# Optimization experiments

Measured on AMD Instinct MI355X. Metric: run time of the kernel, lower is better.

## Reference

```python
import jax, jax.numpy as jnp
import numpy as np

B, S, D, F, E, K, R, H = 4, 1024, 1024, 512, 8, 2, 64, 256
TEMP = 1.0          # step=0 -> 0.5+0.5*cos(0)=1.0, clamp(min=0.1) -> 1.0
BW, EW, ZW = 0.3, 0.1, 1e-4


def fq(t):
    """Per-tensor symmetric int8 fake-quant with straight-through estimator."""
    s = jnp.maximum(jnp.max(jnp.abs(t)) / 127.0, 1e-8)
    q = jnp.clip(jnp.round(t / s), -128, 127) * s
    return t + jax.lax.stop_gradient(q - t)


def lora_lin(h, W, A, Bm):
    # base weight is frozen (requires_grad=False) and fake-quantized
    y = h @ fq(jax.lax.stop_gradient(W)).T + (h @ Bm.T) @ A.T
    return fq(y)


def ffn(h, w1, a1, b1, w2, a2, b2, w3, a3, b3):
    # use_swiglu=True path: gate = sigmoid(w3(x)); out = w2(w1(x)*gate); dropout=eval identity
    gate = jax.nn.sigmoid(lora_lin(h, w3, a3, b3))
    out = lora_lin(lora_lin(h, w1, a1, b1) * gate, w2, a2, b2)
    return fq(out)


def setup_inputs() -> dict:
    key = jax.random.key(0)
    k = jax.random.split(key, 32)
    n = lambda i, shp: jax.random.normal(k[i], shp, dtype=jnp.float32) * 0.02
    return {
        "x": jax.random.normal(k[0], (B, S, D), dtype=jnp.float32),
        "scorer_w": n(1, (E, D)), "scorer_b": jnp.zeros((E,), jnp.float32),
        "p1_w": n(2, (H, D)), "p1_b": jnp.zeros((H,), jnp.float32),
        "p2_w": n(3, (E, H)), "p2_b": jnp.zeros((E,), jnp.float32),
        "ew1_w": n(4, (E, F, D)), "ew1_a": n(5, (E, F, R)), "ew1_b": n(6, (E, R, D)),
        "ew2_w": n(7, (E, D, F)), "ew2_a": n(8, (E, D, R)), "ew2_b": n(9, (E, R, F)),
        "ew3_w": n(10, (E, F, D)), "ew3_a": n(11, (E, F, R)), "ew3_b": n(12, (E, R, D)),
        "s1_w": n(13, (F, D)), "s1_a": n(14, (F, R)), "s1_b": n(15, (R, D)),
        "s2_w": n(16, (D, F)), "s2_a": n(17, (D, R)), "s2_b": n(18, (R, F)),
        "s3_w": n(19, (F, D)), "s3_a": n(20, (F, R)), "s3_b": n(21, (R, D)),
    }


def reference(x, scorer_w, scorer_b, p1_w, p1_b, p2_w, p2_b,
              ew1_w, ew1_a, ew1_b, ew2_w, ew2_a, ew2_b, ew3_w, ew3_a, ew3_b,
              s1_w, s1_a, s1_b, s2_w, s2_a, s2_b, s3_w, s3_a, s3_b):
    xf = x.reshape(-1, D)                                           # [T, D]
    # --- router (per-token) ---
    base = (xf @ scorer_w.T + scorer_b) / TEMP                      # [T, E]
    policy = jax.nn.softmax(jax.nn.relu(xf @ p1_w.T + p1_b) @ p2_w.T + p2_b, axis=-1)
    scores = jax.nn.softmax((base + policy) * 0.5, axis=-1)         # fp32 softmax
    entropy = -(scores * jnp.log(scores + 1e-6)).sum(-1).mean()
    z_loss = ZW * (jax.nn.logsumexp(base, axis=-1) ** 2).mean()
    weights, indices = jax.lax.top_k(scores, K)                     # [T, K]
    weights = weights * TEMP
    cw = (jax.nn.one_hot(indices, E, dtype=weights.dtype) * weights[..., None]).sum(1)  # [T, E]
    usage = cw.sum(0)                                               # [E]
    uf = usage / (usage.mean() + 1e-6)
    balance_loss = BW * jnp.var(uf, ddof=1) - EW * entropy + z_loss
    # --- expert dispatch: dense masked combine (faithful to weighted scatter-add) ---
    eout = jax.vmap(lambda w1, a1, b1, w2, a2, b2, w3, a3, b3:
                    ffn(xf, w1, a1, b1, w2, a2, b2, w3, a3, b3))(
        ew1_w, ew1_a, ew1_b, ew2_w, ew2_a, ew2_b, ew3_w, ew3_a, ew3_b)  # [E, T, D]
    y = jnp.einsum('te,etd->td', cw, eout)                          # weighted combine
    z = ffn(xf, s1_w, s1_a, s1_b, s2_w, s2_a, s2_b, s3_w, s3_a, s3_b)
    out = (y + z).reshape(x.shape)
    return (out, usage, balance_loss, jnp.float32(0.0), jnp.float32(0.0))
```

## Files before the change

### kernel.cpp

```cpp
#include <hip/hip_runtime.h>

#define TTOK 4096
#define DDIM 1024
#define FDIM 512
#define NEXP 8
#define HDIM 256
#define RLORA 64
#define CROWS 14336

using u16 = unsigned short;
using f4v = __attribute__((ext_vector_type(4))) float;
using bfrag = __attribute__((ext_vector_type(8))) short;
using u16x8 = __attribute__((ext_vector_type(8))) unsigned short;

static __device__ __forceinline__ float bf2f(u16 u) {
  union { unsigned int u; float f; } x; x.u = ((unsigned int)u) << 16; return x.f;
}
static __device__ __forceinline__ u16 f2bf(float f) {
  union { float f; unsigned int u; } x; x.f = f;
  unsigned int r = (x.u + 0x7fffu + ((x.u >> 16) & 1u)) >> 16;
  return (u16)r;
}
static __device__ __forceinline__ float fq1(float t, float s) {
  float q = rintf(t / s);
  q = fminf(fmaxf(q, -128.f), 127.f);
  return q * s;
}

struct GemmGArgs {
  const u16* A; const u16* B; u16* C;
  const int* tokmap; const int2* blkmap; const int* nbrow;
};

#define STAGE1(d, kt, h, l) \
  __builtin_amdgcn_global_load_lds( \
    (const __attribute__((address_space(1))) void*)(gs[(h)*2+(l)] + (size_t)(kt)*64), \
    (__attribute__((address_space(3))) void*)&lds[(d)*32768 + (h)*8192 + (tid + (l)*512)*8], \
    16, 0, 0)

template <int MODE>
__global__ __launch_bounds__(512, 2) void gemm256g(GemmGArgs g) {
  const int br = blockIdx.x;
  if (br >= g.nbrow[0]) return;
  const int2 bm = g.blkmap[br];
  const int e = bm.x;
  const int m0 = bm.y;
  const int n0 = blockIdx.y * 256;
  const int tid = threadIdx.x;
  const int lane = tid & 63;
  const int wave = tid >> 6;
  const int wr = wave >> 2;
  const int wc = wave & 3;

  constexpr int K = MODE ? 1024 : 512;
  const u16* Bp = g.B + (size_t)e * (MODE ? 1048576 : 524288);

  __shared__ u16 lds[65536];

  const u16* gs[8];
#pragma unroll
  for (int h = 0; h < 4; h++)
#pragma unroll
    for (int l = 0; l < 2; l++) {
      const int slot = tid + l * 512;
      const int row = slot >> 3, p = slot & 7;
      const int glog = p ^ (row & 7);
      const u16* basep;
      if (h < 2) {
        const int grow = m0 + h * 128 + row;
        const int t = MODE ? g.tokmap[grow] : grow;
        basep = g.A + (size_t)t * K;
      } else {
        basep = Bp + (size_t)(n0 + (h - 2) * 128 + row) * K;
      }
      gs[h * 2 + l] = basep + glog * 8;
    }

  f4v acc[8][4];
#pragma unroll
  for (int i = 0; i < 8; i++)
#pragma unroll
    for (int j = 0; j < 4; j++) acc[i][j] = (f4v){0.f, 0.f, 0.f, 0.f};

  const int q = lane >> 4;
  const int lx = lane & 7;
  const int l15 = lane & 15;

#pragma unroll
  for (int h = 0; h < 4; h++) { STAGE1(0, 0, h, 0); STAGE1(0, 0, h, 1); }
  __syncthreads();

  constexpr int nt = K >> 6;
  for (int kt = 0; kt < nt; ++kt) {
    const int d = kt & 1;
    const int dn = d ^ 1;
    const bool more = (kt + 1 < nt);
#pragma unroll
    for (int kk = 0; kk < 2; ++kk) {
      if (more) {
        if (kk == 0) { STAGE1(dn, kt + 1, 0, 0); STAGE1(dn, kt + 1, 0, 1);
                       STAGE1(dn, kt + 1, 1, 0); STAGE1(dn, kt + 1, 1, 1); }
        else         { STAGE1(dn, kt + 1, 2, 0); STAGE1(dn, kt + 1, 2, 1);
                       STAGE1(dn, kt + 1, 3, 0); STAGE1(dn, kt + 1, 3, 1); }
      }
      bfrag afr[8], bfr[4];
      const int pa = ((kk * 4 + q) ^ lx) << 3;
      const int abase = d * 32768 + wr * 8192 + l15 * 64 + pa;
#pragma unroll
      for (int mi = 0; mi < 8; mi++) afr[mi] = *(const bfrag*)&lds[abase + mi * 1024];
      const int bbase = d * 32768 + (2 + (wc >> 1)) * 8192 + (((wc & 1) << 6) + l15) * 64 + pa;
#pragma unroll
      for (int ni = 0; ni < 4; ni++) bfr[ni] = *(const bfrag*)&lds[bbase + ni * 1024];
      __builtin_amdgcn_s_setprio(1);
#pragma unroll
      for (int mi = 0; mi < 8; mi++)
#pragma unroll
        for (int ni = 0; ni < 4; ni++)
          acc[mi][ni] = __builtin_amdgcn_mfma_f32_16x16x32_bf16(afr[mi], bfr[ni], acc[mi][ni], 0, 0, 0);
      __builtin_amdgcn_s_setprio(0);
    }
    __syncthreads();
  }

  const int crow0 = m0 + wr * 128 + q * 4;

  if (MODE == 1) {
    float* xlds = (float*)lds;
    const int lrow0 = wr * 128 + q * 4;
    if (wc >= 2) {
      const int lc = (wc - 2) * 64 + l15;
#pragma unroll
      for (int mi = 0; mi < 8; mi++)
#pragma unroll
        for (int ni = 0; ni < 4; ni++)
#pragma unroll
          for (int r = 0; r < 4; r++)
            xlds[(lrow0 + mi * 16 + r) * 128 + lc + ni * 16] = acc[mi][ni][r];
    }
    __syncthreads();
    if (wc < 2) {
      const int lc = wc * 64 + l15;
      const int fbase = (n0 >> 1) + lc;
#pragma unroll
      for (int mi = 0; mi < 8; mi++)
#pragma unroll
        for (int r = 0; r < 4; r++) {
          const int rowg = crow0 + mi * 16 + r;
          const int lr = lrow0 + mi * 16 + r;
#pragma unroll
          for (int ni = 0; ni < 4; ni++) {
            float y1 = acc[mi][ni][r];
            float y3 = xlds[lr * 128 + lc + ni * 16];
            float h = y1 / (1.f + __expf(-y3));
            g.C[(size_t)rowg * FDIM + fbase + ni * 16] = f2bf(h);
          }
        }
    }
  } else {
    const int ccol0 = n0 + wc * 64 + l15;
#pragma unroll
    for (int mi = 0; mi < 8; mi++)
#pragma unroll
      for (int ni = 0; ni < 4; ni++) {
        const int col = ccol0 + ni * 16;
#pragma unroll
        for (int r = 0; r < 4; r++)
          g.C[(size_t)(crow0 + mi * 16 + r) * 1024 + col] = f2bf(acc[mi][ni][r]);
      }
  }
}

struct MidArgs {
  const u16* A64; const u16* B64; u16* C64; const float* bias64;
  const u16* A0; const u16* B0;
  const u16* Wb;
  u16* C13; u16* C2e;
  const float* amaxP;
};

__global__ __launch_bounds__(256) void mid_kernel(MidArgs g) {
  __shared__ u16 smem[25600];
  __shared__ float s_sw;
  const int bid = blockIdx.x;
  const int tid = threadIdx.x;
  const int lane = tid & 63;
  const int wave = tid >> 6;

  if (bid < 256) {
    const int wr = wave >> 1, wc = wave & 1;
    const int m0 = (bid & 63) * 64, n0 = (bid >> 6) * 64;
    const int K = DDIM, N = HDIM;
    u16* As = smem;
    u16* Bs = smem + 2048;

    const int ldrow = tid >> 2;
    const int swzcol = (((tid & 3) ^ ((tid >> 3) & 3)) << 3);
    const u16* ga = g.A64 + (size_t)(m0 + ldrow) * K + swzcol;
    const u16* gb = g.B64 + (size_t)(n0 + ldrow) * K + swzcol;

    f4v acc[2][2];
#pragma unroll
    for (int i = 0; i < 2; i++)
#pragma unroll
      for (int j = 0; j < 2; j++) acc[i][j] = (f4v){0.f, 0.f, 0.f, 0.f};

    const int rbase = lane & 15;
    const int q = lane >> 4;
    const int pg = (q ^ ((rbase >> 1) & 3)) << 3;
    const int arow = (wr << 5) + rbase;
    const int brow = (wc << 5) + rbase;

    for (int kt = 0; kt < K; kt += 32) {
      __builtin_amdgcn_global_load_lds((const __attribute__((address_space(1))) void*)(ga),
          (__attribute__((address_space(3))) void*)&As[tid * 8], 16, 0, 0);
      __builtin_amdgcn_global_load_lds((const __attribute__((address_space(1))) void*)(gb),
          (__attribute__((address_space(3))) void*)&Bs[tid * 8], 16, 0, 0);
      ga += 32; gb += 32;
      __syncthreads();
      bfrag af[2], bf[2];
#pragma unroll
      for (int mi = 0; mi < 2; mi++)
        af[mi] = *(const bfrag*)&As[(arow + mi * 16) * 32 + pg];
#pragma unroll
      for (int ni = 0; ni < 2; ni++)
        bf[ni] = *(const bfrag*)&Bs[(brow + ni * 16) * 32 + pg];
#pragma unroll
      for (int mi = 0; mi < 2; mi++)
#pragma unroll
        for (int ni = 0; ni < 2; ni++)
          acc[mi][ni] = __builtin_amdgcn_mfma_f32_16x16x32_bf16(af[mi], bf[ni], acc[mi][ni], 0, 0, 0);
      __syncthreads();
    }

    const int crow0 = m0 + (wr << 5) + ((lane >> 4) << 2);
    const int ccol0 = n0 + (wc << 5) + (lane & 15);
#pragma unroll
    for (int mi = 0; mi < 2; mi++)
#pragma unroll
      for (int ni = 0; ni < 2; ni++) {
        const int n = ccol0 + ni * 16;
        const float b = g.bias64[n];
#pragma unroll
        for (int r = 0; r < 4; r++) {
          float v = fmaxf(acc[mi][ni][r] + b, 0.f);
          g.C64[(size_t)(crow0 + mi * 16 + r) * N + n] = f2bf(v);
        }
      }
    return;
  }

  const int fid = bid - 256;
  const int z = fid >> 6;
  const int rem = fid & 63;
  const int bx = rem & 7, by = rem >> 3;
  const bool is13 = z < 18;
  if (is13 ? (bx >= 4) : (by >= 4)) return;
  const int N = is13 ? 1024 : 512;
  const int K = 64;
  const u16* Ap = is13 ? g.A0 + (size_t)z * 32768 : g.A0 + 589824 + (size_t)(z - 18) * 65536;
  const u16* Bp = is13 ? g.B0 + (size_t)z * 65536 : g.B0 + 1179648 + (size_t)(z - 18) * 32768;
  const u16* Wf = g.Wb + (size_t)z * 524288;
  u16* Cb; int flag;
  if (is13) {
    const int slot = (z >= 16) ? 8 : (z & 7);
    Cb = g.C13 + (size_t)slot * 1048576;
    flag = (z >= 8 && z < 16) || z == 17 ? 2 : 1;
  } else {
    Cb = g.C2e + (size_t)(z - 18) * 524288;
    flag = 0;
  }

  const int wr = wave >> 1, wc = wave & 1;
  const int m0 = bx * 128, n0 = by * 128;
  u16* As = smem;
  u16* Bs = smem + 4096;
  u16* stage = smem + 8192;

  if (wave == 0) {
    float m = fmaxf(g.amaxP[z * 128 + lane], g.amaxP[z * 128 + 64 + lane]);
#pragma unroll
    for (int off = 32; off > 0; off >>= 1) m = fmaxf(m, __shfl_xor(m, off));
    if (lane == 0) s_sw = fmaxf(m / 127.f, 1e-8f);
  }

  const int ldrow = tid >> 2;
  const int swzcol = (((tid & 3) ^ ((tid >> 3) & 3)) << 3);
  const u16* ga = Ap + (size_t)(m0 + ldrow) * K + swzcol;
  const u16* gb = Bp + (size_t)(n0 + ldrow) * K + swzcol;
  const size_t rowstep = (size_t)64 * K;

  f4v acc[4][4];
#pragma unroll
  for (int i = 0; i < 4; i++)
#pragma unroll
    for (int j = 0; j < 4; j++) acc[i][j] = (f4v){0.f, 0.f, 0.f, 0.f};

  const int rbase = lane & 15;
  const int q = lane >> 4;
  const int pg = (q ^ ((rbase >> 1) & 3)) << 3;
  const int arow = (wr << 6) + rbase;
  const int brow = (wc << 6) + rbase;

  for (int kt = 0; kt < K; kt += 32) {
    __builtin_amdgcn_global_load_lds((const __attribute__((address_space(1))) void*)(ga),
        (__attribute__((address_space(3))) void*)&As[tid * 8], 16, 0, 0);
    __builtin_amdgcn_global_load_lds((const __attribute__((address_space(1))) void*)(ga + rowstep),
        (__attribute__((address_space(3))) void*)&As[(256 + tid) * 8], 16, 0, 0);
    __builtin_amdgcn_global_load_lds((const __attribute__((address_space(1))) void*)(gb),
        (__attribute__((address_space(3))) void*)&Bs[tid * 8], 16, 0, 0);
    __builtin_amdgcn_global_load_lds((const __attribute__((address_space(1))) void*)(gb + rowstep),
        (__attribute__((address_space(3))) void*)&Bs[(256 + tid) * 8], 16, 0, 0);
    ga += 32; gb += 32;
    __syncthreads();
    bfrag af[4], bf[4];
#pragma unroll
    for (int mi = 0; mi < 4; mi++)
      af[mi] = *(const bfrag*)&As[(arow + mi * 16) * 32 + pg];
#pragma unroll
    for (int ni = 0; ni < 4; ni++)
      bf[ni] = *(const bfrag*)&Bs[(brow + ni * 16) * 32 + pg];
#pragma unroll
    for (int mi = 0; mi < 4; mi++)
#pragma unroll
      for (int ni = 0; ni < 4; ni++)
        acc[mi][ni] = __builtin_amdgcn_mfma_f32_16x16x32_bf16(af[mi], bf[ni], acc[mi][ni], 0, 0, 0);
    __syncthreads();
  }

  const int lrow0 = (wr << 6) + ((lane >> 4) << 2);
  const int lcol0 = (wc << 6) + (lane & 15);
#pragma unroll
  for (int mi = 0; mi < 4; mi++)
#pragma unroll
    for (int ni = 0; ni < 4; ni++) {
      const int n = lcol0 + ni * 16;
#pragma unroll
      for (int r = 0; r < 4; r++)
        stage[(lrow0 + mi * 16 + r) * 136 + n] = f2bf(acc[mi][ni][r]);
    }
  __syncthreads();
  const float sw = s_sw;

  const int dm0 = flag ? (((m0 >> 7) << 8) + (flag == 2 ? 128 : 0)) : m0;
#pragma unroll
  for (int j = 0; j < 8; j++) {
    const int s = j * 256 + tid;
    const int lr = s >> 4;
    const int n8 = (s & 15) << 3;
    const u16x8 wv = *(const u16x8*)&Wf[(size_t)(m0 + lr) * N + n0 + n8];
    const bfrag sv = *(const bfrag*)&stage[lr * 136 + n8];
    u16x8 o;
#pragma unroll
    for (int k = 0; k < 8; k++)
      o[k] = f2bf(fq1(bf2f(wv[k]), sw) + bf2f((u16)sv[k]));
    *(u16x8*)&Cb[(size_t)(dm0 + lr) * N + n0 + n8] = o;
  }
}

struct PrepArgs {
  const float* W[27]; u16* Wraw; float* amaxP;
  const float* xf; u16* xfb;
  const float* p1w; u16* p1wb;
  const float* Asrc[27]; u16* Adst;
  const float* Bsrc[27]; u16* Bdst;
};
__global__ __launch_bounds__(256) void prep_kernel(PrepArgs a) {
  const int bid = blockIdx.x;
  const int tid = threadIdx.x;
  if (bid < 3456) {
    const int t = bid >> 7;
    const int bx = bid & 127;
    const float4* src = (const float4*)a.W[t];
    ushort4* dst = (ushort4*)(a.Wraw + (size_t)t * 524288);
    const int i0 = bx * 256 + tid;
    float4 v0 = src[i0];
    float4 v1 = src[i0 + 32768];
    float4 v2 = src[i0 + 65536];
    float4 v3 = src[i0 + 98304];
    ushort4 o0, o1, o2, o3;
    o0.x = f2bf(v0.x); o0.y = f2bf(v0.y); o0.z = f2bf(v0.z); o0.w = f2bf(v0.w);
    o1.x = f2bf(v1.x); o1.y = f2bf(v1.y); o1.z = f2bf(v1.z); o1.w = f2bf(v1.w);
    o2.x = f2bf(v2.x); o2.y = f2bf(v2.y); o2.z = f2bf(v2.z); o2.w = f2bf(v2.w);
    o3.x = f2bf(v3.x); o3.y = f2bf(v3.y); o3.z = f2bf(v3.z); o3.w = f2bf(v3.w);
    dst[i0] = o0; dst[i0 + 32768] = o1; dst[i0 + 65536] = o2; dst[i0 + 98304] = o3;
    float m01 = fmaxf(fmaxf(fabsf(v0.x), fabsf(v0.y)), fmaxf(fabsf(v0.z), fabsf(v0.w)));
    float m11 = fmaxf(fmaxf(fabsf(v1.x), fabsf(v1.y)), fmaxf(fabsf(v1.z), fabsf(v1.w)));
    float m21 = fmaxf(fmaxf(fabsf(v2.x), fabsf(v2.y)), fmaxf(fabsf(v2.z), fabsf(v2.w)));
    float m31 = fmaxf(fmaxf(fabsf(v3.x), fabsf(v3.y)), fmaxf(fabsf(v3.z), fabsf(v3.w)));
    float lmax = fmaxf(fmaxf(m01, m11), fmaxf(m21, m31));
#pragma unroll
    for (int off = 32; off > 0; off >>= 1) lmax = fmaxf(lmax, __shfl_xor(lmax, off));
    __shared__ float wm[4];
    if ((tid & 63) == 0) wm[tid >> 6] = lmax;
    __syncthreads();
    if (tid == 0)
      a.amaxP[t * 128 + bx] = fmaxf(fmaxf(wm[0], wm[1]), fmaxf(wm[2], wm[3]));
    return;
  }
  const int cid = bid - 3456;
  const int slice = cid >> 10;
  const int g0 = (cid & 1023) * 256 + tid;
  const int stride = 262144;
  if (slice == 0) {
    for (int i = g0; i < 1048576; i += stride) {
      float4 v = ((const float4*)a.xf)[i];
      ushort4 o; o.x = f2bf(v.x); o.y = f2bf(v.y); o.z = f2bf(v.z); o.w = f2bf(v.w);
      ((ushort4*)a.xfb)[i] = o;
    }
  } else if (slice == 1) {
    for (int i = g0; i < 65536; i += stride) {
      float4 v = ((const float4*)a.p1w)[i];
      ushort4 o; o.x = f2bf(v.x); o.y = f2bf(v.y); o.z = f2bf(v.z); o.w = f2bf(v.w);
      ((ushort4*)a.p1wb)[i] = o;
    }
  } else if (slice == 2) {
    for (int i = g0; i < 1179648; i += stride) {
      int t, off;
      if (i < 589824) { t = i >> 15; off = i & 32767; }
      else { int j = i - 589824; t = 18 + (j >> 16); off = j & 65535; }
      a.Adst[i] = f2bf(a.Asrc[t][off]);
    }
  } else {
    for (int i = g0; i < 1474560; i += stride) {
      int t, src;
      if (i < 1179648) { t = i >> 16; int off = i & 65535; src = (off & 63) * 1024 + (off >> 6); }
      else { int j = i - 1179648; t = 18 + (j >> 15); int off = j & 32767; src = (off & 63) * 512 + (off >> 6); }
      a.Bdst[i] = f2bf(a.Bsrc[t][src]);
    }
  }
}

struct RouterArgs {
  const float* xf; const u16* ph;
  const float* sw; const float* sb;
  const float* p2w; const float* p2b;
  float* base; float* pol;
};
__global__ __launch_bounds__(256) void router_small(RouterArgs a) {
  __shared__ float sw[8][1024];
  __shared__ float p2[8][256];
  const int tid = threadIdx.x;
  {
    const float4* s0 = (const float4*)a.sw;
    float4* d0 = (float4*)&sw[0][0];
    for (int i = tid; i < 2048; i += 256) d0[i] = s0[i];
    const float4* s1 = (const float4*)a.p2w;
    float4* d1 = (float4*)&p2[0][0];
    for (int i = tid; i < 512; i += 256) d1[i] = s1[i];
  }
  __syncthreads();
  const int tl = tid >> 4, s = tid & 15;
  const int token = blockIdx.x * 16 + tl;
  float acc[8] = {0,0,0,0,0,0,0,0}, pacc[8] = {0,0,0,0,0,0,0,0};
  const float4* xrow = (const float4*)(a.xf + (size_t)token * 1024);
  for (int i = 0; i < 16; i++) {
    const int d4 = i * 16 + s;
    float4 xv = xrow[d4];
#pragma unroll
    for (int e = 0; e < 8; e++) {
      float4 wv = ((const float4*)&sw[e][0])[d4];
      acc[e] += xv.x * wv.x + xv.y * wv.y + xv.z * wv.z + xv.w * wv.w;
    }
  }
  const u16* phrow = a.ph + (size_t)token * 256;
  for (int i = 0; i < 16; i++) {
    const int h = i * 16 + s;
    float pv = bf2f(phrow[h]);
#pragma unroll
    for (int e = 0; e < 8; e++) pacc[e] += pv * p2[e][h];
  }
#pragma unroll
  for (int off = 8; off > 0; off >>= 1)
#pragma unroll
    for (int e = 0; e < 8; e++) {
      acc[e] += __shfl_xor(acc[e], off);
      pacc[e] += __shfl_xor(pacc[e], off);
    }
  if (s == 0) {
#pragma unroll
    for (int e = 0; e < 8; e++) {
      a.base[token * 8 + e] = acc[e] + a.sb[e];
      a.pol[token * 8 + e] = pacc[e] + a.p2b[e];
    }
  }
}

struct FinArgs {
  const float* base; const float* pol;
  float* partials;
  int* idx2; float2* wb; int* histArr;
};
__global__ __launch_bounds__(256) void router_topk(FinArgs a) {
  const int tid = threadIdx.x;
  const int lane = tid & 63, wv = tid >> 6;
  const int token = blockIdx.x * 256 + tid;
  float b[8], p[8];
#pragma unroll
  for (int e = 0; e < 8; e++) { b[e] = a.base[token * 8 + e]; p[e] = a.pol[token * 8 + e]; }
  float pm = p[0];
#pragma unroll
  for (int e = 1; e < 8; e++) pm = fmaxf(pm, p[e]);
  float pe[8], psum = 0.f;
#pragma unroll
  for (int e = 0; e < 8; e++) { pe[e] = expf(p[e] - pm); psum += pe[e]; }
  const float pinv = 1.f / psum;
  float sl[8];
#pragma unroll
  for (int e = 0; e < 8; e++) sl[e] = (b[e] + pe[e] * pinv) * 0.5f;
  float sm = sl[0];
#pragma unroll
  for (int e = 1; e < 8; e++) sm = fmaxf(sm, sl[e]);
  float sc[8], ssum = 0.f;
#pragma unroll
  for (int e = 0; e < 8; e++) { sc[e] = expf(sl[e] - sm); ssum += sc[e]; }
  const float sinv = 1.f / ssum;
  float ent = 0.f;
#pragma unroll
  for (int e = 0; e < 8; e++) { float v = sc[e] * sinv; sc[e] = v; ent -= v * logf(v + 1e-6f); }
  float bm = b[0];
#pragma unroll
  for (int e = 1; e < 8; e++) bm = fmaxf(bm, b[e]);
  float zs = 0.f;
#pragma unroll
  for (int e = 0; e < 8; e++) zs += expf(b[e] - bm);
  const float lse = logf(zs) + bm;
  const float zt = lse * lse;
  float m1 = -1e30f, m2 = -1e30f; int i1 = 0, i2 = 0;
#pragma unroll
  for (int e = 0; e < 8; e++) {
    float v = sc[e];
    if (v > m1) { m2 = m1; i2 = i1; m1 = v; i1 = e; }
    else if (v > m2) { m2 = v; i2 = e; }
  }
  a.idx2[token] = i1 | (i2 << 8);
  a.wb[token] = make_float2(m1, m2);

  __shared__ int hist[8];
  if (tid < 8) hist[tid] = 0;
  __syncthreads();
  atomicAdd(&hist[i1], 1);
  atomicAdd(&hist[i2], 1);
  __syncthreads();
  if (tid < 8) a.histArr[blockIdx.x * 8 + tid] = hist[tid];

  float vals[10];
  vals[0] = ent; vals[1] = zt;
#pragma unroll
  for (int e = 0; e < 8; e++) vals[2 + e] = 0.f;
  vals[2 + i1] = m1; vals[2 + i2] = m2;
#pragma unroll
  for (int v = 0; v < 10; v++)
#pragma unroll
    for (int off = 32; off > 0; off >>= 1) vals[v] += __shfl_down(vals[v], off);
  __shared__ float wred[4][10];
  if (lane == 0)
#pragma unroll
    for (int v = 0; v < 10; v++) wred[wv][v] = vals[v];
  __syncthreads();
  if (tid < 10)
    a.partials[blockIdx.x * 10 + tid] = wred[0][tid] + wred[1][tid] + wred[2][tid] + wred[3][tid];
}

__global__ __launch_bounds__(256) void compact_setup(const int* idx2, const int* histArr,
                                                     int2* blkmap, int* nbrow, int* tokmap,
                                                     int* posb, const float* partials, float* tail) {
  const int e = blockIdx.x;
  const int tid = threadIdx.x;
  int cntl[8];
#pragma unroll
  for (int i = 0; i < 8; i++) {
    int s = 0;
    for (int bblk = 0; bblk < 16; bblk++) s += histArr[bblk * 8 + i];
    cntl[i] = s;
  }
  if (e == 8) {
    if (tid == 0) {
      int o = 0, nb = 16;
      for (int i = 0; i < 16; i++) blkmap[i] = make_int2(8, i * 256);
      for (int ex = 0; ex < 8; ex++) {
        const int nbe = (cntl[ex] + 255) >> 8;
        for (int i = 0; i < nbe; i++) blkmap[nb++] = make_int2(ex, 4096 + o + i * 256);
        o += nbe << 8;
      }
      nbrow[0] = nb;
    } else if (tid == 64) {
      float ent = 0.f, z = 0.f, us[8] = {0,0,0,0,0,0,0,0};
      for (int i = 0; i < 16; i++) {
        ent += partials[i * 10 + 0];
        z += partials[i * 10 + 1];
        for (int ex = 0; ex < 8; ex++) us[ex] += partials[i * 10 + 2 + ex];
      }
      float tot = 0.f;
      for (int ex = 0; ex < 8; ex++) tot += us[ex];
      const float meanu = tot / 8.f;
      float uf[8], mu = 0.f;
      for (int ex = 0; ex < 8; ex++) { uf[ex] = us[ex] / (meanu + 1e-6f); mu += uf[ex]; }
      mu /= 8.f;
      float var = 0.f;
      for (int ex = 0; ex < 8; ex++) { float d = uf[ex] - mu; var += d * d; }
      var /= 7.f;
      const float bl = 0.3f * var - 0.1f * (ent / 4096.f) + 1e-4f * (z / 4096.f);
      for (int ex = 0; ex < 8; ex++) tail[ex] = us[ex];
      tail[8] = bl; tail[9] = 0.f; tail[10] = 0.f;
    }
    for (int t = tid; t < 4096; t += 256) tokmap[t] = t;
    return;
  }
  const int lane = tid & 63, wv = tid >> 6;
  __shared__ int wtot[4];
  __shared__ int carry;
  if (tid == 0) carry = 0;
  __syncthreads();
  int off = 0;
  for (int i = 0; i < e; i++) off += ((cntl[i] + 255) >> 8) << 8;
  const int base = 4096 + off;
  for (int c = 0; c < 16; c++) {
    const int t = c * 256 + tid;
    const int ii = idx2[t];
    const int i1 = ii & 255, i2 = ii >> 8;
    const int flag = (i1 == e || i2 == e) ? 1 : 0;
    const unsigned long long m = __ballot(flag);
    const int pre = __popcll(m & ((1ull << lane) - 1ull));
    if (lane == 63) wtot[wv] = pre + flag;
    __syncthreads();
    int wbase = 0;
    for (int i = 0; i < wv; i++) wbase += wtot[i];
    if (flag) {
      const int row = base + carry + wbase + pre;
      tokmap[row] = t;
      posb[t * 2 + (i2 == e ? 1 : 0)] = row;
    }
    __syncthreads();
    if (tid == 0) carry += wtot[0] + wtot[1] + wtot[2] + wtot[3];
    __syncthreads();
  }
  const int ce = cntl[e];
  const int pend = ((ce + 255) >> 8) << 8;
  for (int r = ce + tid; r < pend; r += 256) tokmap[base + r] = 0;
}

__global__ __launch_bounds__(256) void combine_g(const u16* y2c, const int* posb,
                                                 const float2* wb, float* out) {
  const int t = blockIdx.x;
  const int c = threadIdx.x;
  const float2 w = wb[t];
  const int p1 = posb[t * 2], p2 = posb[t * 2 + 1];
  ushort4 s = ((const ushort4*)(y2c + (size_t)t * 1024))[c];
  ushort4 a = ((const ushort4*)(y2c + (size_t)p1 * 1024))[c];
  ushort4 b = ((const ushort4*)(y2c + (size_t)p2 * 1024))[c];
  float4 o;
  o.x = bf2f(s.x) + w.x * bf2f(a.x) + w.y * bf2f(b.x);
  o.y = bf2f(s.y) + w.x * bf2f(a.y) + w.y * bf2f(b.y);
  o.z = bf2f(s.z) + w.x * bf2f(a.z) + w.y * bf2f(b.z);
  o.w = bf2f(s.w) + w.x * bf2f(a.w) + w.y * bf2f(b.w);
  ((float4*)(out + (size_t)t * 1024))[c] = o;
}

extern "C" void kernel_launch(void* const* d_in, const int* in_sizes, int n_in,
                              void* d_out, int out_size, void* d_ws, size_t ws_size,
                              hipStream_t stream) {
  const float* x = (const float*)d_in[0];
  const float* scorer_w = (const float*)d_in[1];
  const float* scorer_b = (const float*)d_in[2];
  const float* p1_w = (const float*)d_in[3];
  const float* p1_b = (const float*)d_in[4];
  const float* p2_w = (const float*)d_in[5];
  const float* p2_b = (const float*)d_in[6];
  const float* ew1_w = (const float*)d_in[7];
  const float* ew1_a = (const float*)d_in[8];
  const float* ew1_b = (const float*)d_in[9];
  const float* ew2_w = (const float*)d_in[10];
  const float* ew2_a = (const float*)d_in[11];
  const float* ew2_b = (const float*)d_in[12];
  const float* ew3_w = (const float*)d_in[13];
  const float* ew3_a = (const float*)d_in[14];
  const float* ew3_b = (const float*)d_in[15];
  const float* s1_w = (const float*)d_in[16];
  const float* s1_a = (const float*)d_in[17];
  const float* s1_b = (const float*)d_in[18];
  const float* s2_w = (const float*)d_in[19];
  const float* s2_a = (const float*)d_in[20];
  const float* s2_b = (const float*)d_in[21];
  const float* s3_w = (const float*)d_in[22];
  const float* s3_a = (const float*)d_in[23];
  const float* s3_b = (const float*)d_in[24];
  float* outf = (float*)d_out;

  char* w = (char*)d_ws;
  auto alloc = [&](size_t bytes) { char* p = w; w += (bytes + 255) & ~(size_t)255; return p; };
  u16* xfb  = (u16*)alloc((size_t)TTOK * DDIM * 2);
  u16* ph   = (u16*)alloc((size_t)TTOK * HDIM * 2);
  u16* p1wb = (u16*)alloc((size_t)HDIM * DDIM * 2);
  u16* Adst = (u16*)alloc((size_t)1179648 * 2);
  u16* Bdst = (u16*)alloc((size_t)1474560 * 2);
  u16* Wraw = (u16*)alloc((size_t)27 * 524288 * 2);
  u16* W13  = (u16*)alloc((size_t)9 * 1024 * 1024 * 2);
  u16* W2e  = (u16*)alloc((size_t)9 * 1024 * 512 * 2);
  u16* h2c  = (u16*)alloc((size_t)CROWS * FDIM * 2);
  u16* y2c  = (u16*)alloc((size_t)CROWS * DDIM * 2);
  float* base = (float*)alloc((size_t)TTOK * 8 * 4);
  float* pol  = (float*)alloc((size_t)TTOK * 8 * 4);
  float* partials = (float*)alloc(16 * 10 * 4);
  float* amaxP = (float*)alloc(27 * 128 * 4);
  int* histArr = (int*)alloc(16 * 8 * 4);
  int2* blkmap = (int2*)alloc(64 * 8);
  int* nbrow  = (int*)alloc(4);
  int* tokmap = (int*)alloc(CROWS * 4);
  int* posb   = (int*)alloc(TTOK * 2 * 4);
  int* idx2   = (int*)alloc(TTOK * 4);
  float2* wb  = (float2*)alloc(TTOK * 8);

  {
    PrepArgs a{};
    for (int e = 0; e < 8; e++) {
      a.W[e] = ew1_w + (size_t)e * 524288;
      a.W[8 + e] = ew3_w + (size_t)e * 524288;
      a.W[18 + e] = ew2_w + (size_t)e * 524288;
      a.Asrc[e] = ew1_a + (size_t)e * 32768;
      a.Asrc[8 + e] = ew3_a + (size_t)e * 32768;
      a.Asrc[18 + e] = ew2_a + (size_t)e * 65536;
      a.Bsrc[e] = ew1_b + (size_t)e * 65536;
      a.Bsrc[8 + e] = ew3_b + (size_t)e * 65536;
      a.Bsrc[18 + e] = ew2_b + (size_t)e * 32768;
    }
    a.W[16] = s1_w; a.W[17] = s3_w; a.W[26] = s2_w;
    a.Asrc[16] = s1_a; a.Asrc[17] = s3_a; a.Asrc[26] = s2_a;
    a.Bsrc[16] = s1_b; a.Bsrc[17] = s3_b; a.Bsrc[26] = s2_b;
    a.Wraw = Wraw; a.amaxP = amaxP;
    a.xf = x; a.xfb = xfb; a.p1w = p1_w; a.p1wb = p1wb;
    a.Adst = Adst; a.Bdst = Bdst;
    hipLaunchKernelGGL(prep_kernel, dim3(7552), dim3(256), 0, stream, a);
  }
  {
    MidArgs g{};
    g.A64 = xfb; g.B64 = p1wb; g.C64 = ph; g.bias64 = p1_b;
    g.A0 = Adst; g.B0 = Bdst; g.Wb = Wraw; g.C13 = W13; g.C2e = W2e; g.amaxP = amaxP;
    hipLaunchKernelGGL(mid_kernel, dim3(1984), dim3(256), 0, stream, g);
  }
  {
    RouterArgs r{};
    r.xf = x; r.ph = ph; r.sw = scorer_w; r.sb = scorer_b;
    r.p2w = p2_w; r.p2b = p2_b; r.base = base; r.pol = pol;
    hipLaunchKernelGGL(router_small, dim3(256), dim3(256), 0, stream, r);
  }
  {
    FinArgs f{base, pol, partials, idx2, wb, histArr};
    hipLaunchKernelGGL(router_topk, dim3(16), dim3(256), 0, stream, f);
  }
  hipLaunchKernelGGL(compact_setup, dim3(9), dim3(256), 0, stream,
                     idx2, histArr, blkmap, nbrow, tokmap, posb, partials,
                     outf + (size_t)TTOK * DDIM);
  {
    GemmGArgs g{xfb, W13, h2c, tokmap, blkmap, nbrow};
    hipLaunchKernelGGL(gemm256g<1>, dim3(56, 4), dim3(512), 0, stream, g);
  }
  {
    GemmGArgs g{h2c, W2e, y2c, tokmap, blkmap, nbrow};
    hipLaunchKernelGGL(gemm256g<0>, dim3(56, 4), dim3(512), 0, stream, g);
  }
  hipLaunchKernelGGL(combine_g, dim3(4096), dim3(256), 0, stream, y2c, posb, wb, outf);
}
```

Baseline: 153.3 us.

## Fuse router kernels, remap GEMM block order, stage gate tile in bf16

Merges the router logit kernel and the top-k/softmax kernel into one launch. Logits now stay in shared memory, which drops the base/pol global round trip and one kernel launch. In exchange, the partial sums and histograms grow to 256 blocks, so compact_setup reduces more entries. The GEMMs use a 1D grid with a remapped block order so that the four column tiles of a row block land on the same XCD, aiming at better L2 reuse. The gate tile staged in LDS becomes bf16 with a padded stride of 136, which halves LDS traffic but rounds the gate logits to bf16 before the sigmoid.

Result: slower. 222.0 us (+44.7%).

```diff
diff --git a/kernel.cpp b/kernel.cpp
--- a/kernel.cpp
+++ b/kernel.cpp
@@ -40,12 +40,14 @@
 
 template <int MODE>
 __global__ __launch_bounds__(512, 2) void gemm256g(GemmGArgs g) {
-  const int br = blockIdx.x;
+  const int bid = blockIdx.x;
+  const int logical = (bid & 7) * 28 + (bid >> 3);
+  const int br = logical >> 2;
   if (br >= g.nbrow[0]) return;
   const int2 bm = g.blkmap[br];
   const int e = bm.x;
   const int m0 = bm.y;
-  const int n0 = blockIdx.y * 256;
+  const int n0 = (logical & 3) * 256;
   const int tid = threadIdx.x;
   const int lane = tid & 63;
   const int wave = tid >> 6;
@@ -125,7 +127,7 @@
   const int crow0 = m0 + wr * 128 + q * 4;
 
   if (MODE == 1) {
-    float* xlds = (float*)lds;
+    u16* stage = lds;
     const int lrow0 = wr * 128 + q * 4;
     if (wc >= 2) {
       const int lc = (wc - 2) * 64 + l15;
@@ -135,7 +137,7 @@
         for (int ni = 0; ni < 4; ni++)
 #pragma unroll
           for (int r = 0; r < 4; r++)
-            xlds[(lrow0 + mi * 16 + r) * 128 + lc + ni * 16] = acc[mi][ni][r];
+            stage[(lrow0 + mi * 16 + r) * 136 + lc + ni * 16] = f2bf(acc[mi][ni][r]);
     }
     __syncthreads();
     if (wc < 2) {
@@ -150,7 +152,7 @@
 #pragma unroll
           for (int ni = 0; ni < 4; ni++) {
             float y1 = acc[mi][ni][r];
-            float y3 = xlds[lr * 128 + lc + ni * 16];
+            float y3 = bf2f(stage[lr * 136 + lc + ni * 16]);
             float h = y1 / (1.f + __expf(-y3));
             g.C[(size_t)rowg * FDIM + fbase + ni * 16] = f2bf(h);
           }
@@ -434,11 +436,16 @@
   const float* xf; const u16* ph;
   const float* sw; const float* sb;
   const float* p2w; const float* p2b;
-  float* base; float* pol;
+  int* idx2; float2* wb;
+  float* partials;
+  int* histArr;
 };
-__global__ __launch_bounds__(256) void router_small(RouterArgs a) {
+__global__ __launch_bounds__(256) void router_kernel(RouterArgs a) {
   __shared__ float sw[8][1024];
   __shared__ float p2[8][256];
+  __shared__ float blog[16][8];
+  __shared__ float plog[16][8];
+  __shared__ int hist[8];
   const int tid = threadIdx.x;
   {
     const float4* s0 = (const float4*)a.sw;
@@ -448,117 +455,106 @@
     float4* d1 = (float4*)&p2[0][0];
     for (int i = tid; i < 512; i += 256) d1[i] = s1[i];
   }
+  if (tid < 8) hist[tid] = 0;
   __syncthreads();
   const int tl = tid >> 4, s = tid & 15;
   const int token = blockIdx.x * 16 + tl;
-  float acc[8] = {0,0,0,0,0,0,0,0}, pacc[8] = {0,0,0,0,0,0,0,0};
-  const float4* xrow = (const float4*)(a.xf + (size_t)token * 1024);
-  for (int i = 0; i < 16; i++) {
-    const int d4 = i * 16 + s;
-    float4 xv = xrow[d4];
+  {
+    float acc[8] = {0,0,0,0,0,0,0,0}, pacc[8] = {0,0,0,0,0,0,0,0};
+    const float4* xrow = (const float4*)(a.xf + (size_t)token * 1024);
+    for (int i = 0; i < 16; i++) {
+      const int d4 = i * 16 + s;
+      float4 xv = xrow[d4];
+#pragma unroll
+      for (int e = 0; e < 8; e++) {
+        float4 wv = ((const float4*)&sw[e][0])[d4];
+        acc[e] += xv.x * wv.x + xv.y * wv.y + xv.z * wv.z + xv.w * wv.w;
+      }
+    }
+    const u16* phrow = a.ph + (size_t)token * 256;
+    for (int i = 0; i < 16; i++) {
+      const int h = i * 16 + s;
+      float pv = bf2f(phrow[h]);
+#pragma unroll
+      for (int e = 0; e < 8; e++) pacc[e] += pv * p2[e][h];
+    }
+#pragma unroll
+    for (int off = 8; off > 0; off >>= 1)
+#pragma unroll
+      for (int e = 0; e < 8; e++) {
+        acc[e] += __shfl_xor(acc[e], off);
+        pacc[e] += __shfl_xor(pacc[e], off);
+      }
+    if (s == 0) {
+#pragma unroll
+      for (int e = 0; e < 8; e++) {
+        blog[tl][e] = acc[e] + a.sb[e];
+        plog[tl][e] = pacc[e] + a.p2b[e];
+      }
+    }
+  }
+  __syncthreads();
+
+  float vals[10];
+#pragma unroll
+  for (int v = 0; v < 10; v++) vals[v] = 0.f;
+  if (tid < 16) {
+    const int tok = blockIdx.x * 16 + tid;
+    float b[8], p[8];
+#pragma unroll
+    for (int e = 0; e < 8; e++) { b[e] = blog[tid][e]; p[e] = plog[tid][e]; }
+    float pm = p[0];
+#pragma unroll
+    for (int e = 1; e < 8; e++) pm = fmaxf(pm, p[e]);
+    float pe[8], psum = 0.f;
+#pragma unroll
+    for (int e = 0; e < 8; e++) { pe[e] = expf(p[e] - pm); psum += pe[e]; }
+    const float pinv = 1.f / psum;
+    float sl[8];
+#pragma unroll
+    for (int e = 0; e < 8; e++) sl[e] = (b[e] + pe[e] * pinv) * 0.5f;
+    float sm = sl[0];
+#pragma unroll
+    for (int e = 1; e < 8; e++) sm = fmaxf(sm, sl[e]);
+    float sc[8], ssum = 0.f;
+#pragma unroll
+    for (int e = 0; e < 8; e++) { sc[e] = expf(sl[e] - sm); ssum += sc[e]; }
+    const float sinv = 1.f / ssum;
+    float ent = 0.f;
+#pragma unroll
+    for (int e = 0; e < 8; e++) { float v = sc[e] * sinv; sc[e] = v; ent -= v * logf(v + 1e-6f); }
+    float bm = b[0];
+#pragma unroll
+    for (int e = 1; e < 8; e++) bm = fmaxf(bm, b[e]);
+    float zs = 0.f;
+#pragma unroll
+    for (int e = 0; e < 8; e++) zs += expf(b[e] - bm);
+    const float lse = logf(zs) + bm;
+    float m1 = -1e30f, m2 = -1e30f; int i1 = 0, i2 = 0;
 #pragma unroll
     for (int e = 0; e < 8; e++) {
-      float4 wv = ((const float4*)&sw[e][0])[d4];
-      acc[e] += xv.x * wv.x + xv.y * wv.y + xv.z * wv.z + xv.w * wv.w;
-    }
-  }
-  const u16* phrow = a.ph + (size_t)token * 256;
-  for (int i = 0; i < 16; i++) {
-    const int h = i * 16 + s;
-    float pv = bf2f(phrow[h]);
-#pragma unroll
-    for (int e = 0; e < 8; e++) pacc[e] += pv * p2[e][h];
-  }
-#pragma unroll
-  for (int off = 8; off > 0; off >>= 1)
-#pragma unroll
-    for (int e = 0; e < 8; e++) {
-      acc[e] += __shfl_xor(acc[e], off);
-      pacc[e] += __shfl_xor(pacc[e], off);
-    }
-  if (s == 0) {
-#pragma unroll
-    for (int e = 0; e < 8; e++) {
-      a.base[token * 8 + e] = acc[e] + a.sb[e];
-      a.pol[token * 8 + e] = pacc[e] + a.p2b[e];
-    }
-  }
-}
-
-struct FinArgs {
-  const float* base; const float* pol;
-  float* partials;
-  int* idx2; float2* wb; int* histArr;
-};
-__global__ __launch_bounds__(256) void router_topk(FinArgs a) {
-  const int tid = threadIdx.x;
-  const int lane = tid & 63, wv = tid >> 6;
-  const int token = blockIdx.x * 256 + tid;
-  float b[8], p[8];
-#pragma unroll
-  for (int e = 0; e < 8; e++) { b[e] = a.base[token * 8 + e]; p[e] = a.pol[token * 8 + e]; }
-  float pm = p[0];
-#pragma unroll
-  for (int e = 1; e < 8; e++) pm = fmaxf(pm, p[e]);
-  float pe[8], psum = 0.f;
-#pragma unroll
-  for (int e = 0; e < 8; e++) { pe[e] = expf(p[e] - pm); psum += pe[e]; }
-  const float pinv = 1.f / psum;
-  float sl[8];
-#pragma unroll
-  for (int e = 0; e < 8; e++) sl[e] = (b[e] + pe[e] * pinv) * 0.5f;
-  float sm = sl[0];
-#pragma unroll
-  for (int e = 1; e < 8; e++) sm = fmaxf(sm, sl[e]);
-  float sc[8], ssum = 0.f;
-#pragma unroll
-  for (int e = 0; e < 8; e++) { sc[e] = expf(sl[e] - sm); ssum += sc[e]; }
-  const float sinv = 1.f / ssum;
-  float ent = 0.f;
-#pragma unroll
-  for (int e = 0; e < 8; e++) { float v = sc[e] * sinv; sc[e] = v; ent -= v * logf(v + 1e-6f); }
-  float bm = b[0];
-#pragma unroll
-  for (int e = 1; e < 8; e++) bm = fmaxf(bm, b[e]);
-  float zs = 0.f;
-#pragma unroll
-  for (int e = 0; e < 8; e++) zs += expf(b[e] - bm);
-  const float lse = logf(zs) + bm;
-  const float zt = lse * lse;
-  float m1 = -1e30f, m2 = -1e30f; int i1 = 0, i2 = 0;
-#pragma unroll
-  for (int e = 0; e < 8; e++) {
-    float v = sc[e];
-    if (v > m1) { m2 = m1; i2 = i1; m1 = v; i1 = e; }
-    else if (v > m2) { m2 = v; i2 = e; }
-  }
-  a.idx2[token] = i1 | (i2 << 8);
-  a.wb[token] = make_float2(m1, m2);
-
-  __shared__ int hist[8];
-  if (tid < 8) hist[tid] = 0;
-  __syncthreads();
-  atomicAdd(&hist[i1], 1);
-  atomicAdd(&hist[i2], 1);
+      float v = sc[e];
+      if (v > m1) { m2 = m1; i2 = i1; m1 = v; i1 = e; }
+      else if (v > m2) { m2 = v; i2 = e; }
+    }
+    a.idx2[tok] = i1 | (i2 << 8);
+    a.wb[tok] = make_float2(m1, m2);
+    atomicAdd(&hist[i1], 1);
+    atomicAdd(&hist[i2], 1);
+    vals[0] = ent; vals[1] = lse * lse;
+    vals[2 + i1] = m1; vals[2 + i2] = m2;
+  }
+  if (tid < 64) {
+#pragma unroll
+    for (int v = 0; v < 10; v++)
+#pragma unroll
+      for (int off = 32; off > 0; off >>= 1) vals[v] += __shfl_down(vals[v], off);
+    if (tid == 0)
+#pragma unroll
+      for (int v = 0; v < 10; v++) a.partials[blockIdx.x * 10 + v] = vals[v];
+  }
   __syncthreads();
   if (tid < 8) a.histArr[blockIdx.x * 8 + tid] = hist[tid];
-
-  float vals[10];
-  vals[0] = ent; vals[1] = zt;
-#pragma unroll
-  for (int e = 0; e < 8; e++) vals[2 + e] = 0.f;
-  vals[2 + i1] = m1; vals[2 + i2] = m2;
-#pragma unroll
-  for (int v = 0; v < 10; v++)
-#pragma unroll
-    for (int off = 32; off > 0; off >>= 1) vals[v] += __shfl_down(vals[v], off);
-  __shared__ float wred[4][10];
-  if (lane == 0)
-#pragma unroll
-    for (int v = 0; v < 10; v++) wred[wv][v] = vals[v];
-  __syncthreads();
-  if (tid < 10)
-    a.partials[blockIdx.x * 10 + tid] = wred[0][tid] + wred[1][tid] + wred[2][tid] + wred[3][tid];
 }
 
 __global__ __launch_bounds__(256) void compact_setup(const int* idx2, const int* histArr,
@@ -570,7 +566,7 @@
 #pragma unroll
   for (int i = 0; i < 8; i++) {
     int s = 0;
-    for (int bblk = 0; bblk < 16; bblk++) s += histArr[bblk * 8 + i];
+    for (int bblk = 0; bblk < 256; bblk++) s += histArr[bblk * 8 + i];
     cntl[i] = s;
   }
   if (e == 8) {
@@ -585,7 +581,7 @@
       nbrow[0] = nb;
     } else if (tid == 64) {
       float ent = 0.f, z = 0.f, us[8] = {0,0,0,0,0,0,0,0};
-      for (int i = 0; i < 16; i++) {
+      for (int i = 0; i < 256; i++) {
         ent += partials[i * 10 + 0];
         z += partials[i * 10 + 1];
         for (int ex = 0; ex < 8; ex++) us[ex] += partials[i * 10 + 2 + ex];
@@ -698,11 +694,9 @@
   u16* W2e  = (u16*)alloc((size_t)9 * 1024 * 512 * 2);
   u16* h2c  = (u16*)alloc((size_t)CROWS * FDIM * 2);
   u16* y2c  = (u16*)alloc((size_t)CROWS * DDIM * 2);
-  float* base = (float*)alloc((size_t)TTOK * 8 * 4);
-  float* pol  = (float*)alloc((size_t)TTOK * 8 * 4);
-  float* partials = (float*)alloc(16 * 10 * 4);
+  float* partials = (float*)alloc(256 * 10 * 4);
   float* amaxP = (float*)alloc(27 * 128 * 4);
-  int* histArr = (int*)alloc(16 * 8 * 4);
+  int* histArr = (int*)alloc(256 * 8 * 4);
   int2* blkmap = (int2*)alloc(64 * 8);
   int* nbrow  = (int*)alloc(4);
   int* tokmap = (int*)alloc(CROWS * 4);
@@ -740,23 +734,20 @@
   {
     RouterArgs r{};
     r.xf = x; r.ph = ph; r.sw = scorer_w; r.sb = scorer_b;
-    r.p2w = p2_w; r.p2b = p2_b; r.base = base; r.pol = pol;
-    hipLaunchKernelGGL(router_small, dim3(256), dim3(256), 0, stream, r);
-  }
-  {
-    FinArgs f{base, pol, partials, idx2, wb, histArr};
-    hipLaunchKernelGGL(router_topk, dim3(16), dim3(256), 0, stream, f);
+    r.p2w = p2_w; r.p2b = p2_b;
+    r.idx2 = idx2; r.wb = wb; r.partials = partials; r.histArr = histArr;
+    hipLaunchKernelGGL(router_kernel, dim3(256), dim3(256), 0, stream, r);
   }
   hipLaunchKernelGGL(compact_setup, dim3(9), dim3(256), 0, stream,
                      idx2, histArr, blkmap, nbrow, tokmap, posb, partials,
                      outf + (size_t)TTOK * DDIM);
   {
     GemmGArgs g{xfb, W13, h2c, tokmap, blkmap, nbrow};
-    hipLaunchKernelGGL(gemm256g<1>, dim3(56, 4), dim3(512), 0, stream, g);
+    hipLaunchKernelGGL(gemm256g<1>, dim3(224), dim3(512), 0, stream, g);
   }
   {
     GemmGArgs g{h2c, W2e, y2c, tokmap, blkmap, nbrow};
-    hipLaunchKernelGGL(gemm256g<0>, dim3(56, 4), dim3(512), 0, stream, g);
+    hipLaunchKernelGGL(gemm256g<0>, dim3(224), dim3(512), 0, stream, g);
   }
   hipLaunchKernelGGL(combine_g, dim3(4096), dim3(256), 0, stream, y2c, posb, wb, outf);
 }
```
